# Optimization experiments

Hardware: AMD Instinct MI355X
Metric: run time of the kernel (lower is better)

## Reference

```python
import jax, jax.numpy as jnp
import numpy as np

B, T, D = 4, 2048, 1024
H, DH = 16, 64
GH = H * DH  # == D here
SCALE = DH ** -0.5
LN_EPS = 1e-5


def setup_inputs() -> dict:
    key = jax.random.key(0)
    ks = jax.random.split(key, 8)
    x = jax.random.normal(ks[0], (B, T, D), dtype=jnp.float32)
    attn_mask = jax.random.uniform(ks[1], (T, T), dtype=jnp.float32)
    # LayerNorm params
    gamma = jnp.ones((D,), jnp.float32)
    beta = jnp.zeros((D,), jnp.float32)
    # projection weights, stored (in, out) so y = x @ W
    Wq = jax.random.normal(ks[2], (D, GH), jnp.float32) * (D ** -0.5)
    Wk = jax.random.normal(ks[3], (D, GH), jnp.float32) * (D ** -0.5)
    Wv = jax.random.normal(ks[4], (D, GH), jnp.float32) * (D ** -0.5)
    Wo = jax.random.normal(ks[5], (GH, D), jnp.float32) * (GH ** -0.5)
    bo = jnp.zeros((D,), jnp.float32)
    return {"x": x, "attn_mask": attn_mask, "gamma": gamma, "beta": beta,
            "Wq": Wq, "Wk": Wk, "Wv": Wv, "Wo": Wo, "bo": bo}


def reference(x, attn_mask, gamma, beta, Wq, Wk, Wv, Wo, bo):
    # LayerNorm over last dim
    mu = jnp.mean(x, axis=-1, keepdims=True)
    var = jnp.mean((x - mu) ** 2, axis=-1, keepdims=True)
    xn = (x - mu) * jax.lax.rsqrt(var + LN_EPS) * gamma + beta
    # QKV projections (bias=False), reshape to [B, H, T, DH]
    split = lambda y: y.reshape(B, T, H, DH).transpose(0, 2, 1, 3)
    q = split(xn @ Wq)
    k = split(xn @ Wk)
    v = split(xn @ Wv)
    # scores scaled then MULTIPLICATIVELY masked (post-scale)
    scores = jnp.einsum('bhqd,bhkd->bhqk', q, k) * SCALE
    scores = scores * attn_mask  # broadcast [T,T] over [B,H,T,T]
    probs = jax.nn.softmax(scores, axis=-1)  # dropout p=0 -> identity
    av = jnp.einsum('bhqk,bhkd->bhqd', probs, v)
    av = av.transpose(0, 2, 1, 3).reshape(B, T, GH)
    return av @ Wo + bo
```

## Files before the change

### kernel.cpp

```cpp
#include <hip/hip_runtime.h>

typedef unsigned short u16;
typedef unsigned int u32;
typedef __bf16 bf16x8 __attribute__((ext_vector_type(8)));
typedef float f32x4 __attribute__((ext_vector_type(4)));

#define AS1 __attribute__((address_space(1)))
#define AS3 __attribute__((address_space(3)))

#define SWZB(x) ((x) ^ ((((x) >> 7) & 7) << 4))

__device__ __forceinline__ float bf2f(u16 u) {
    union { u32 i; float f; } v; v.i = ((u32)u) << 16; return v.f;
}
__device__ __forceinline__ u16 f2bf(float f) {
    union { float f; u32 i; } v; v.f = f;
    u32 i = v.i;
    u32 r = (i + 0x7fffu + ((i >> 16) & 1u)) >> 16;
    return (u16)r;
}
__device__ __forceinline__ u32 cvtpk_bf16(float lo, float hi) {
    u32 r;
    asm("v_cvt_pk_bf16_f32 %0, %1, %2" : "=v"(r) : "v"(lo), "v"(hi));
    return r;
}
__device__ __forceinline__ void gload_lds16(const u16* src, u16* dst) {
    __builtin_amdgcn_global_load_lds((const AS1 void*)src, (AS3 void*)dst, 16, 0, 0);
}

__global__ __launch_bounds__(256) void transpose1024(const float* __restrict__ in,
                                                     u16* __restrict__ out,
                                                     float scale) {
    __shared__ u16 t[64][65];
    int c = threadIdx.x & 63, r0 = threadIdx.x >> 6;
    int ib = blockIdx.y * 64, jb = blockIdx.x * 64;
    #pragma unroll
    for (int r = r0; r < 64; r += 4)
        t[r][c] = f2bf(in[(size_t)(ib + r) * 1024 + jb + c] * scale);
    __syncthreads();
    #pragma unroll
    for (int r = r0; r < 64; r += 4) out[(size_t)(jb + r) * 1024 + ib + c] = t[c][r];
}

__global__ __launch_bounds__(256) void vtrans(const u16* __restrict__ qkv,
                                              u16* __restrict__ vT) {
    int bh = blockIdx.y, b = bh >> 4, h = bh & 15;
    int t0 = blockIdx.x * 64;
    __shared__ u16 tl[64][65];
    int c = threadIdx.x & 63, r0 = threadIdx.x >> 6;
    const u16* src = qkv + ((size_t)(b * 2048 + t0)) * 3072 + 2048 + h * 64;
    #pragma unroll
    for (int r = r0; r < 64; r += 4) tl[r][c] = src[(size_t)r * 3072 + c];
    __syncthreads();
    u16* dst = vT + ((size_t)bh * 64) * 2048 + t0;
    #pragma unroll
    for (int r = r0; r < 64; r += 4) dst[(size_t)r * 2048 + c] = tl[c][r];
}

__global__ __launch_bounds__(256) void ln_kernel(const float* __restrict__ x,
                                                 const float* __restrict__ g,
                                                 const float* __restrict__ bb,
                                                 u16* __restrict__ xn) {
    int row = blockIdx.x;
    int tid = threadIdx.x;
    const float* xr = x + (size_t)row * 1024;
    float4 v = *(const float4*)&xr[tid * 4];
    float f0 = v.x, f1 = v.y, f2 = v.z, f3 = v.w;
    float s = f0 + f1 + f2 + f3;
    float sq = f0 * f0 + f1 * f1 + f2 * f2 + f3 * f3;
    #pragma unroll
    for (int m = 1; m < 64; m <<= 1) { s += __shfl_xor(s, m, 64); sq += __shfl_xor(sq, m, 64); }
    __shared__ float red[8];
    int wid = tid >> 6, lane = tid & 63;
    if (lane == 0) { red[wid] = s; red[4 + wid] = sq; }
    __syncthreads();
    s = red[0] + red[1] + red[2] + red[3];
    sq = red[4] + red[5] + red[6] + red[7];
    float mu = s * (1.f / 1024.f);
    float var = sq * (1.f / 1024.f) - mu * mu;
    float rs = rsqrtf(var + 1e-5f);
    float4 gv = *(const float4*)&g[tid * 4];
    float4 bv = *(const float4*)&bb[tid * 4];
    ushort4 o;
    o.x = f2bf((f0 - mu) * rs * gv.x + bv.x);
    o.y = f2bf((f1 - mu) * rs * gv.y + bv.y);
    o.z = f2bf((f2 - mu) * rs * gv.z + bv.z);
    o.w = f2bf((f3 - mu) * rs * gv.w + bv.w);
    *(ushort4*)&xn[(size_t)row * 1024 + tid * 4] = o;
}

__global__ __launch_bounds__(256) void gemm_bt(const u16* __restrict__ A,
                                               const u16* __restrict__ BT,
                                               u16* __restrict__ C16,
                                               float* __restrict__ C32,
                                               const float* __restrict__ bias,
                                               int K, int ldc, int ext) {
    __shared__ __align__(16) u16 lA[128 * 32];
    __shared__ __align__(16) u16 lB[128 * 32];
    int tid = threadIdx.x, lane = tid & 63, wid = tid >> 6;
    int wr = wid >> 1, wc = wid & 1;
    int m0 = blockIdx.y * 128, n0 = blockIdx.x * 128;
    int l4 = lane >> 4, l15 = lane & 15;

    f32x4 acc[4][4] = {};
    int NT = K >> 5;

    auto stage = [&](int kt) {
        int k0 = kt << 5;
        #pragma unroll
        for (int i = 0; i < 2; ++i) {
            int j = wid * 2 + i;
            int row = j * 16 + (lane >> 2);
            int ch = (lane & 3) * 8;
            gload_lds16(A + (size_t)(m0 + row) * K + k0 + ch, &lA[j * 512]);
            gload_lds16(BT + (size_t)(n0 + row) * K + k0 + ch, &lB[j * 512]);
        }
    };
    stage(0);
    for (int kt = 0; kt < NT; ++kt) {
        __syncthreads();
        bf16x8 af[4], bfr[4];
        #pragma unroll
        for (int i = 0; i < 4; ++i) {
            af[i]  = *(const bf16x8*)&lA[(wr * 64 + i * 16 + l15) * 32 + l4 * 8];
            bfr[i] = *(const bf16x8*)&lB[(wc * 64 + i * 16 + l15) * 32 + l4 * 8];
        }
        __syncthreads();
        if (kt + 1 < NT) stage(kt + 1);
        #pragma unroll
        for (int i = 0; i < 4; ++i)
            #pragma unroll
            for (int j = 0; j < 4; ++j)
                acc[i][j] = __builtin_amdgcn_mfma_f32_16x16x32_bf16(af[i], bfr[j], acc[i][j], 0, 0, 0);
    }
    #pragma unroll
    for (int j = 0; j < 4; ++j) {
        int col = n0 + wc * 64 + j * 16 + l15;
        float bv = ext ? bias[col] : 0.f;
        #pragma unroll
        for (int i = 0; i < 4; ++i) {
            #pragma unroll
            for (int r = 0; r < 4; ++r) {
                int row = m0 + wr * 64 + i * 16 + l4 * 4 + r;
                float val = acc[i][j][r] + bv;
                if (ext) C32[(size_t)row * ldc + col] = val;
                else     C16[(size_t)row * ldc + col] = f2bf(val);
            }
        }
    }
}

__global__ __launch_bounds__(256) void attn_kernel(const u16* __restrict__ qkv,
                                                   const u16* __restrict__ vT,
                                                   const float* __restrict__ mask,
                                                   u16* __restrict__ av) {
    __shared__ __align__(16) u16 lK[2][64 * 64];
    __shared__ __align__(16) u16 lV[2][64 * 64];
    int qt = blockIdx.x, bh = blockIdx.y;
    int b = bh >> 4, h = bh & 15;
    int tid = threadIdx.x, lane = tid & 63, wid = tid >> 6;
    int l4 = lane >> 4, l15 = lane & 15;
    int qw = qt * 128 + wid * 32;

    const u16* qb0 = qkv + (size_t)(b * 2048 + qw + l15) * 3072 + h * 64;
    const u16* qb1 = qb0 + (size_t)16 * 3072;
    bf16x8 qf00 = *(const bf16x8*)&qb0[l4 * 8];
    bf16x8 qf01 = *(const bf16x8*)&qb0[32 + l4 * 8];
    bf16x8 qf10 = *(const bf16x8*)&qb1[l4 * 8];
    bf16x8 qf11 = *(const bf16x8*)&qb1[32 + l4 * 8];
    const float* mrow0 = mask + (size_t)(qw + l15) * 2048 + 8 * l4;
    const float* mrow1 = mrow0 + (size_t)16 * 2048;

    f32x4 o0[4] = {}, o1[4] = {};
    float lsum0 = 0.f, lsum1 = 0.f;

    int c0 = tid, c1 = 256 + tid;
    auto pmap = [](int g) {
        return (g & 32) + 4 * ((g >> 3) & 3) + (g & 3) + ((g & 4) << 2);
    };
    int kd0 = SWZB(pmap(c0 >> 3) * 128 + (c0 & 7) * 16);
    int kd1 = SWZB(pmap(c1 >> 3) * 128 + (c1 & 7) * 16);
    int vd0 = SWZB((c0 >> 3) * 128 + (c0 & 7) * 16);
    int vd1 = SWZB((c1 >> 3) * 128 + (c1 & 7) * 16);
    const u16* ksrc0 = qkv + (size_t)(b * 2048 + (c0 >> 3)) * 3072 + 1024 + h * 64 + (c0 & 7) * 8;
    const u16* ksrc1 = qkv + (size_t)(b * 2048 + (c1 >> 3)) * 3072 + 1024 + h * 64 + (c1 & 7) * 8;
    const u16* vsrc0 = vT + (size_t)(bh * 64 + (c0 >> 3)) * 2048 + (c0 & 7) * 8;
    const u16* vsrc1 = vT + (size_t)(bh * 64 + (c1 >> 3)) * 2048 + (c1 & 7) * 8;

    auto loadKV = [&](int t, bf16x8& K0, bf16x8& K1, bf16x8& V0, bf16x8& V1) {
        size_t ko = (size_t)t * (64 * 3072);
        int vo = t * 64;
        K0 = *(const bf16x8*)(ksrc0 + ko);
        K1 = *(const bf16x8*)(ksrc1 + ko);
        V0 = *(const bf16x8*)(vsrc0 + vo);
        V1 = *(const bf16x8*)(vsrc1 + vo);
    };

    union PU { u32 u[4]; bf16x8 v; };

    auto body = [&](int t, int pbuf,
                    bf16x8& cK0, bf16x8& cK1, bf16x8& cV0, bf16x8& cV1,
                    bf16x8& nK0, bf16x8& nK1, bf16x8& nV0, bf16x8& nV1) {
        *(bf16x8*)((char*)lK[pbuf] + kd0) = cK0;
        *(bf16x8*)((char*)lK[pbuf] + kd1) = cK1;
        *(bf16x8*)((char*)lV[pbuf] + vd0) = cV0;
        *(bf16x8*)((char*)lV[pbuf] + vd1) = cV1;
        __syncthreads();
        if (t + 1 < 32) loadKV(t + 1, nK0, nK1, nV0, nV1);
        int k0 = t * 64;
        f32x4 mm0[4], mm1[4];
        mm0[0] = *(const f32x4*)(mrow0 + k0);
        mm0[1] = *(const f32x4*)(mrow0 + k0 + 4);
        mm0[2] = *(const f32x4*)(mrow0 + k0 + 32);
        mm0[3] = *(const f32x4*)(mrow0 + k0 + 36);
        mm1[0] = *(const f32x4*)(mrow1 + k0);
        mm1[1] = *(const f32x4*)(mrow1 + k0 + 4);
        mm1[2] = *(const f32x4*)(mrow1 + k0 + 32);
        mm1[3] = *(const f32x4*)(mrow1 + k0 + 36);
        const char* Kb = (const char*)lK[pbuf];
        f32x4 s0[4] = {}, s1[4] = {};
        __builtin_amdgcn_s_setprio(1);
        #pragma unroll
        for (int fj = 0; fj < 4; ++fj) {
            bf16x8 kf0 = *(const bf16x8*)(Kb + SWZB((fj * 16 + l15) * 128 + l4 * 16));
            bf16x8 kf1 = *(const bf16x8*)(Kb + SWZB((fj * 16 + l15) * 128 + 64 + l4 * 16));
            s0[fj] = __builtin_amdgcn_mfma_f32_16x16x32_bf16(kf0, qf00, s0[fj], 0, 0, 0);
            s0[fj] = __builtin_amdgcn_mfma_f32_16x16x32_bf16(kf1, qf01, s0[fj], 0, 0, 0);
            s1[fj] = __builtin_amdgcn_mfma_f32_16x16x32_bf16(kf0, qf10, s1[fj], 0, 0, 0);
            s1[fj] = __builtin_amdgcn_mfma_f32_16x16x32_bf16(kf1, qf11, s1[fj], 0, 0, 0);
        }
        __builtin_amdgcn_s_setprio(0);
        PU pa0[2], pa1[2];
        #pragma unroll
        for (int fj = 0; fj < 4; ++fj) {
            float p0 = __expf(s0[fj][0] * mm0[fj][0]);
            float p1 = __expf(s0[fj][1] * mm0[fj][1]);
            float p2 = __expf(s0[fj][2] * mm0[fj][2]);
            float p3 = __expf(s0[fj][3] * mm0[fj][3]);
            lsum0 += (p0 + p1) + (p2 + p3);
            int ks = fj >> 1, hf = (fj & 1) * 2;
            pa0[ks].u[hf]     = cvtpk_bf16(p0, p1);
            pa0[ks].u[hf + 1] = cvtpk_bf16(p2, p3);
        }
        #pragma unroll
        for (int fj = 0; fj < 4; ++fj) {
            float p0 = __expf(s1[fj][0] * mm1[fj][0]);
            float p1 = __expf(s1[fj][1] * mm1[fj][1]);
            float p2 = __expf(s1[fj][2] * mm1[fj][2]);
            float p3 = __expf(s1[fj][3] * mm1[fj][3]);
            lsum1 += (p0 + p1) + (p2 + p3);
            int ks = fj >> 1, hf = (fj & 1) * 2;
            pa1[ks].u[hf]     = cvtpk_bf16(p0, p1);
            pa1[ks].u[hf + 1] = cvtpk_bf16(p2, p3);
        }
        const char* Vb = (const char*)lV[pbuf];
        __builtin_amdgcn_s_setprio(1);
        #pragma unroll
        for (int ks = 0; ks < 2; ++ks) {
            #pragma unroll
            for (int fj = 0; fj < 4; ++fj) {
                bf16x8 vf = *(const bf16x8*)(Vb + SWZB((fj * 16 + l15) * 128 + ks * 64 + l4 * 16));
                o0[fj] = __builtin_amdgcn_mfma_f32_16x16x32_bf16(pa0[ks].v, vf, o0[fj], 0, 0, 0);
                o1[fj] = __builtin_amdgcn_mfma_f32_16x16x32_bf16(pa1[ks].v, vf, o1[fj], 0, 0, 0);
            }
        }
        __builtin_amdgcn_s_setprio(0);
    };

    bf16x8 ka0, ka1, va0, va1, kb0, kb1, vb0, vb1;
    loadKV(0, ka0, ka1, va0, va1);
    for (int t = 0; t < 32; t += 2) {
        body(t,     0, ka0, ka1, va0, va1, kb0, kb1, vb0, vb1);
        body(t + 1, 1, kb0, kb1, vb0, vb1, ka0, ka1, va0, va1);
    }

    lsum0 += __shfl_xor(lsum0, 16, 64);
    lsum0 += __shfl_xor(lsum0, 32, 64);
    lsum1 += __shfl_xor(lsum1, 16, 64);
    lsum1 += __shfl_xor(lsum1, 32, 64);
    float den0[4], den1[4];
    #pragma unroll
    for (int r = 0; r < 4; ++r) {
        den0[r] = __shfl(lsum0, l4 * 4 + r, 64);
        den1[r] = __shfl(lsum1, l4 * 4 + r, 64);
    }
    #pragma unroll
    for (int fj = 0; fj < 4; ++fj) {
        #pragma unroll
        for (int r = 0; r < 4; ++r) {
            int col = h * 64 + fj * 16 + l15;
            av[(size_t)(b * 2048 + qw + l4 * 4 + r) * 1024 + col]      = f2bf(o0[fj][r] / den0[r]);
            av[(size_t)(b * 2048 + qw + 16 + l4 * 4 + r) * 1024 + col] = f2bf(o1[fj][r] / den1[r]);
        }
    }
}

extern "C" void kernel_launch(void* const* d_in, const int* in_sizes, int n_in,
                              void* d_out, int out_size, void* d_ws, size_t ws_size,
                              hipStream_t stream) {
    (void)in_sizes; (void)n_in; (void)out_size; (void)ws_size;
    const float* x     = (const float*)d_in[0];
    const float* mask  = (const float*)d_in[1];
    const float* gamma = (const float*)d_in[2];
    const float* beta  = (const float*)d_in[3];
    const float* Wq    = (const float*)d_in[4];
    const float* Wk    = (const float*)d_in[5];
    const float* Wv    = (const float*)d_in[6];
    const float* Wo    = (const float*)d_in[7];
    const float* bo    = (const float*)d_in[8];

    char* ws = (char*)d_ws;
    u16* xn   = (u16*)(ws);
    u16* WT   = (u16*)(ws + 16777216);
    u16* WoT  = (u16*)(ws + 16777216 + 6291456);
    u16* qkvb = (u16*)(ws + 16777216 + 6291456 + 2097152);
    u16* vT   = (u16*)(ws + 16777216 + 6291456 + 2097152 + 50331648);
    u16* av = xn;

    dim3 tb(256);
    transpose1024<<<dim3(16, 16), tb, 0, stream>>>(Wq, WT, 0.125f);
    transpose1024<<<dim3(16, 16), tb, 0, stream>>>(Wk, WT + 1024 * 1024, 1.0f);
    transpose1024<<<dim3(16, 16), tb, 0, stream>>>(Wv, WT + 2 * 1024 * 1024, 1.0f);
    transpose1024<<<dim3(16, 16), tb, 0, stream>>>(Wo, WoT, 1.0f);
    ln_kernel<<<8192, tb, 0, stream>>>(x, gamma, beta, xn);
    gemm_bt<<<dim3(24, 64), tb, 0, stream>>>(xn, WT, qkvb, nullptr, nullptr, 1024, 3072, 0);
    vtrans<<<dim3(32, 64), tb, 0, stream>>>(qkvb, vT);
    attn_kernel<<<dim3(16, 64), tb, 0, stream>>>(qkvb, vT, mask, av);
    gemm_bt<<<dim3(8, 64), tb, 0, stream>>>(av, WoT, nullptr, (float*)d_out, bo, 1024, 1024, 1);
}
```

Measured before the change: 284.0 us.

## Prefetch K/V two tiles ahead in attention and fold log2e into Q scale

Restructures the attention loop so the next tile's K/V registers are written to the alternate LDS buffer mid-iteration, and the global load for tile t+2 is issued before the PV MFMAs. There is now one barrier per iteration, placed at the end. Separately, log2(e) is folded into the Wq scale so softmax can use raw v_exp_f32 instead of __expf, dropping a multiply per element. This adds register pressure from a deeper prefetch and changes the order of the barriers.

```diff
diff --git a/kernel.cpp b/kernel.cpp
--- a/kernel.cpp
+++ b/kernel.cpp
@@ -22,6 +22,11 @@
 __device__ __forceinline__ u32 cvtpk_bf16(float lo, float hi) {
     u32 r;
     asm("v_cvt_pk_bf16_f32 %0, %1, %2" : "=v"(r) : "v"(lo), "v"(hi));
+    return r;
+}
+__device__ __forceinline__ float fexp2(float x) {
+    float r;
+    asm("v_exp_f32 %0, %1" : "=v"(r) : "v"(x));
     return r;
 }
 __device__ __forceinline__ void gload_lds16(const u16* src, u16* dst) {
@@ -199,14 +204,8 @@
     union PU { u32 u[4]; bf16x8 v; };
 
     auto body = [&](int t, int pbuf,
-                    bf16x8& cK0, bf16x8& cK1, bf16x8& cV0, bf16x8& cV1,
-                    bf16x8& nK0, bf16x8& nK1, bf16x8& nV0, bf16x8& nV1) {
-        *(bf16x8*)((char*)lK[pbuf] + kd0) = cK0;
-        *(bf16x8*)((char*)lK[pbuf] + kd1) = cK1;
-        *(bf16x8*)((char*)lV[pbuf] + vd0) = cV0;
-        *(bf16x8*)((char*)lV[pbuf] + vd1) = cV1;
-        __syncthreads();
-        if (t + 1 < 32) loadKV(t + 1, nK0, nK1, nV0, nV1);
+                    bf16x8& nK0, bf16x8& nK1, bf16x8& nV0, bf16x8& nV1,
+                    bf16x8& fK0, bf16x8& fK1, bf16x8& fV0, bf16x8& fV1) {
         int k0 = t * 64;
         f32x4 mm0[4], mm1[4];
         mm0[0] = *(const f32x4*)(mrow0 + k0);
@@ -233,10 +232,10 @@
         PU pa0[2], pa1[2];
         #pragma unroll
         for (int fj = 0; fj < 4; ++fj) {
-            float p0 = __expf(s0[fj][0] * mm0[fj][0]);
-            float p1 = __expf(s0[fj][1] * mm0[fj][1]);
-            float p2 = __expf(s0[fj][2] * mm0[fj][2]);
-            float p3 = __expf(s0[fj][3] * mm0[fj][3]);
+            float p0 = fexp2(s0[fj][0] * mm0[fj][0]);
+            float p1 = fexp2(s0[fj][1] * mm0[fj][1]);
+            float p2 = fexp2(s0[fj][2] * mm0[fj][2]);
+            float p3 = fexp2(s0[fj][3] * mm0[fj][3]);
             lsum0 += (p0 + p1) + (p2 + p3);
             int ks = fj >> 1, hf = (fj & 1) * 2;
             pa0[ks].u[hf]     = cvtpk_bf16(p0, p1);
@@ -244,15 +243,24 @@
         }
         #pragma unroll
         for (int fj = 0; fj < 4; ++fj) {
-            float p0 = __expf(s1[fj][0] * mm1[fj][0]);
-            float p1 = __expf(s1[fj][1] * mm1[fj][1]);
-            float p2 = __expf(s1[fj][2] * mm1[fj][2]);
-            float p3 = __expf(s1[fj][3] * mm1[fj][3]);
+            float p0 = fexp2(s1[fj][0] * mm1[fj][0]);
+            float p1 = fexp2(s1[fj][1] * mm1[fj][1]);
+            float p2 = fexp2(s1[fj][2] * mm1[fj][2]);
+            float p3 = fexp2(s1[fj][3] * mm1[fj][3]);
             lsum1 += (p0 + p1) + (p2 + p3);
             int ks = fj >> 1, hf = (fj & 1) * 2;
             pa1[ks].u[hf]     = cvtpk_bf16(p0, p1);
             pa1[ks].u[hf + 1] = cvtpk_bf16(p2, p3);
         }
+        if (t + 1 < 32) {
+            char* Kn = (char*)lK[pbuf ^ 1];
+            char* Vn = (char*)lV[pbuf ^ 1];
+            *(bf16x8*)(Kn + kd0) = nK0;
+            *(bf16x8*)(Kn + kd1) = nK1;
+            *(bf16x8*)(Vn + vd0) = nV0;
+            *(bf16x8*)(Vn + vd1) = nV1;
+        }
+        if (t + 2 < 32) loadKV(t + 2, fK0, fK1, fV0, fV1);
         const char* Vb = (const char*)lV[pbuf];
         __builtin_amdgcn_s_setprio(1);
         #pragma unroll
@@ -265,13 +273,20 @@
             }
         }
         __builtin_amdgcn_s_setprio(0);
+        __syncthreads();
     };
 
     bf16x8 ka0, ka1, va0, va1, kb0, kb1, vb0, vb1;
     loadKV(0, ka0, ka1, va0, va1);
+    *(bf16x8*)((char*)lK[0] + kd0) = ka0;
+    *(bf16x8*)((char*)lK[0] + kd1) = ka1;
+    *(bf16x8*)((char*)lV[0] + vd0) = va0;
+    *(bf16x8*)((char*)lV[0] + vd1) = va1;
+    loadKV(1, kb0, kb1, vb0, vb1);
+    __syncthreads();
     for (int t = 0; t < 32; t += 2) {
-        body(t,     0, ka0, ka1, va0, va1, kb0, kb1, vb0, vb1);
-        body(t + 1, 1, kb0, kb1, vb0, vb1, ka0, ka1, va0, va1);
+        body(t,     0, kb0, kb1, vb0, vb1, ka0, ka1, va0, va1);
+        body(t + 1, 1, ka0, ka1, va0, va1, kb0, kb1, vb0, vb1);
     }
 
     lsum0 += __shfl_xor(lsum0, 16, 64);
@@ -318,7 +333,7 @@
     u16* av = xn;
 
     dim3 tb(256);
-    transpose1024<<<dim3(16, 16), tb, 0, stream>>>(Wq, WT, 0.125f);
+    transpose1024<<<dim3(16, 16), tb, 0, stream>>>(Wq, WT, 0.18033688f);
     transpose1024<<<dim3(16, 16), tb, 0, stream>>>(Wk, WT + 1024 * 1024, 1.0f);
     transpose1024<<<dim3(16, 16), tb, 0, stream>>>(Wv, WT + 2 * 1024 * 1024, 1.0f);
     transpose1024<<<dim3(16, 16), tb, 0, stream>>>(Wo, WoT, 1.0f);
```

After: 280.3 us. Within noise of the previous version (-1.3%).
